# Kernel optimization log

Measured on AMD Instinct MI355X. Metric: run time of the kernel, lower is better.

Reference implementation:

```python
import jax, jax.numpy as jnp
import numpy as np

B, L, D, H, BS, R, MLP = 2, 4096, 768, 12, 64, 3, 3072
HD = D // H            # 64 head dim
NB = L // BS           # 64 blocks
EPS = 1e-6
SEED = 0               # connectivity_seed


def _rand_plan():
    """Static BigBird key-block plan for middle query blocks: [NB-2, 5+R].
    Columns: global first, global last, window (i-1, i, i+1), R random blocks."""
    rng = np.random.RandomState(SEED)
    rows = []
    for i in range(1, NB - 1):
        excl = {0, NB - 1, i - 1, i, i + 1}
        cand = np.array([j for j in range(NB) if j not in excl])
        rnd = rng.choice(cand, size=R, replace=False)
        rows.append(np.concatenate([np.array([0, NB - 1, i - 1, i, i + 1]), rnd]))
    return jnp.asarray(np.stack(rows), dtype=jnp.int32)

_PLAN = _rand_plan()


def _layernorm(x, scale, bias):
    mu = jnp.mean(x, axis=-1, keepdims=True)
    var = jnp.mean(jnp.square(x - mu), axis=-1, keepdims=True)
    return (x - mu) * jax.lax.rsqrt(var + EPS) * scale + bias


def _bigbird_attention(x, Wq, Wk, Wv, Wo):
    # projections: [B,L,D] x [D,H,HD] -> [B,H,L,HD]; flax scales q by 1/sqrt(HD)
    q = jnp.einsum('bld,dhk->bhlk', x, Wq) / jnp.sqrt(jnp.asarray(HD, x.dtype))
    k = jnp.einsum('bld,dhk->bhlk', x, Wk)
    v = jnp.einsum('bld,dhk->bhlk', x, Wv)
    qb = q.reshape(B, H, NB, BS, HD)
    kb = k.reshape(B, H, NB, BS, HD)
    vb = v.reshape(B, H, NB, BS, HD)
    # global query rows (first & last block) attend densely to all keys
    qg = qb[:, :, jnp.array([0, NB - 1])]                 # [B,H,2,BS,HD]
    sg = jnp.einsum('bhgqd,bhld->bhgql', qg, k)           # [B,H,2,BS,L]
    og = jnp.einsum('bhgql,bhld->bhgqd', jax.nn.softmax(sg, axis=-1), v)
    # middle query rows: gather window + global + random key blocks
    S = _PLAN.shape[1]                                     # 5 + R = 8 blocks
    km = kb[:, :, _PLAN].reshape(B, H, NB - 2, S * BS, HD)
    vm = vb[:, :, _PLAN].reshape(B, H, NB - 2, S * BS, HD)
    sm = jnp.einsum('bhmqd,bhmkd->bhmqk', qb[:, :, 1:NB - 1], km)
    om = jnp.einsum('bhmqk,bhmkd->bhmqd', jax.nn.softmax(sm, axis=-1), vm)
    ob = jnp.concatenate([og[:, :, :1], om, og[:, :, 1:]], axis=2)  # [B,H,NB,BS,HD]
    o = ob.reshape(B, H, L, HD)
    return jnp.einsum('bhlk,hkd->bld', o, Wo)


def setup_inputs() -> dict:
    key = jax.random.key(0)
    ks = jax.random.split(key, 8)
    s_qkv = (2.0 / (D + HD)) ** 0.5   # xavier-uniform-ish std
    s_mlp1 = (2.0 / (D + MLP)) ** 0.5
    return {
        'x': jax.random.normal(ks[0], (B, L, D), jnp.float32),
        'ln1_scale': jnp.ones((D,), jnp.float32),
        'ln1_bias': jnp.zeros((D,), jnp.float32),
        'Wq': jax.random.normal(ks[1], (D, H, HD), jnp.float32) * s_qkv,
        'Wk': jax.random.normal(ks[2], (D, H, HD), jnp.float32) * s_qkv,
        'Wv': jax.random.normal(ks[3], (D, H, HD), jnp.float32) * s_qkv,
        'Wo': jax.random.normal(ks[4], (H, HD, D), jnp.float32) * s_qkv,
        'ln2_scale': jnp.ones((D,), jnp.float32),
        'ln2_bias': jnp.zeros((D,), jnp.float32),
        'W1': jax.random.normal(ks[5], (D, MLP), jnp.float32) * s_mlp1,
        'b1': jnp.zeros((MLP,), jnp.float32),
        'W2': jax.random.normal(ks[6], (MLP, D), jnp.float32) * s_mlp1,
        'b2': jnp.zeros((D,), jnp.float32),
    }


def reference(x, ln1_scale, ln1_bias, Wq, Wk, Wv, Wo, ln2_scale, ln2_bias, W1, b1, W2, b2):
    h = _layernorm(x, ln1_scale, ln1_bias)
    attn = _bigbird_attention(h, Wq, Wk, Wv, Wo)
    x1 = attn + x                                  # residual (dropout deterministic)
    y = _layernorm(x1, ln2_scale, ln2_bias)
    y = jax.nn.relu(jnp.einsum('bld,df->blf', y, W1) + b1)
    y = jnp.einsum('blf,fd->bld', y, W2) + b2
    return x1 + y
```

## Files before the change

kernel.cpp:

```cpp
#include <hip/hip_runtime.h>
#include <stdint.h>

constexpr int D_MODEL = 768;
constexpr int SEQ     = 4096;
constexpr int NHEAD   = 12;
constexpr int HDIM    = 64;
constexpr int BATCH   = 2;
constexpr int DFF     = 3072;
constexpr int ROWS    = BATCH * SEQ;

typedef __attribute__((ext_vector_type(8))) __bf16 bfrag;
typedef __attribute__((ext_vector_type(8))) short  s16x8;
typedef __attribute__((ext_vector_type(4))) short  s16x4;
typedef __attribute__((ext_vector_type(4))) float  f32x4;

#define MFMA16(a, b, c) __builtin_amdgcn_mfma_f32_16x16x32_bf16((a), (b), (c), 0, 0, 0)
#define AS1(p) ((__attribute__((address_space(1))) void*)(uintptr_t)(p))
#define AS3(p) ((__attribute__((address_space(3))) void*)(p))

__device__ __forceinline__ float b2f(short s) {
  union { unsigned u; float f; } c;
  c.u = ((unsigned)(unsigned short)s) << 16;
  return c.f;
}
__device__ __forceinline__ short f2b(float f) {
  union { float f; unsigned u; } c;
  c.f = f;
  unsigned r = c.u + 0x7fffu + ((c.u >> 16) & 1u);
  return (short)(r >> 16);
}

struct PlanT { int v[64][8]; };

struct MTRng {
  unsigned mt[624];
  int mti;
  constexpr MTRng() : mt{}, mti(624) {
    mt[0] = 0u;
    for (int i = 1; i < 624; ++i)
      mt[i] = 1812433253u * (mt[i-1] ^ (mt[i-1] >> 30)) + (unsigned)i;
  }
  constexpr unsigned next() {
    if (mti >= 624) {
      for (int i = 0; i < 624; ++i) {
        unsigned y = (mt[i] & 0x80000000u) | (mt[(i+1) % 624] & 0x7fffffffu);
        unsigned v = mt[(i+397) % 624] ^ (y >> 1);
        if (y & 1u) v ^= 0x9908b0dfu;
        mt[i] = v;
      }
      mti = 0;
    }
    unsigned y = mt[mti++];
    y ^= y >> 11;
    y ^= (y << 7)  & 0x9d2c5680u;
    y ^= (y << 15) & 0xefc60000u;
    y ^= y >> 18;
    return y;
  }
  constexpr unsigned interval(unsigned mx) {
    unsigned mask = mx;
    mask |= mask >> 1; mask |= mask >> 2; mask |= mask >> 4;
    mask |= mask >> 8; mask |= mask >> 16;
    unsigned v = next() & mask;
    while (v > mx) v = next() & mask;
    return v;
  }
};

constexpr PlanT make_plan() {
  PlanT P{};
  MTRng rng{};
  for (int i = 1; i <= 62; ++i) {
    int cand[64] = {}; int n = 0;
    for (int j = 0; j < 64; ++j) {
      if (j == 0 || j == 63 || j == i-1 || j == i || j == i+1) continue;
      cand[n++] = j;
    }
    int perm[64] = {};
    for (int p = 0; p < n; ++p) perm[p] = p;
    for (int p = n - 1; p > 0; --p) {
      int j = (int)rng.interval((unsigned)p);
      int t = perm[p]; perm[p] = perm[j]; perm[j] = t;
    }
    P.v[i][0] = 0;  P.v[i][1] = 63; P.v[i][2] = i-1; P.v[i][3] = i; P.v[i][4] = i+1;
    P.v[i][5] = cand[perm[0]]; P.v[i][6] = cand[perm[1]]; P.v[i][7] = cand[perm[2]];
  }
  return P;
}
constexpr PlanT h_plan = make_plan();
__constant__ PlanT g_plan = h_plan;

__global__ __launch_bounds__(256) void ln_kernel(
    const float* __restrict__ x, const float* __restrict__ sc,
    const float* __restrict__ bi, short* __restrict__ y)
{
  const int row = blockIdx.x, tid = threadIdx.x;
  const size_t base = (size_t)row * D_MODEL;
  float v0 = x[base + tid], v1 = x[base + tid + 256], v2 = x[base + tid + 512];
  float s  = v0 + v1 + v2;
  float s2 = v0*v0 + v1*v1 + v2*v2;
  for (int off = 1; off < 64; off <<= 1) {
    s  += __shfl_xor(s,  off);
    s2 += __shfl_xor(s2, off);
  }
  __shared__ float red[8];
  if ((tid & 63) == 0) { red[tid >> 6] = s; red[4 + (tid >> 6)] = s2; }
  __syncthreads();
  s  = red[0] + red[1] + red[2] + red[3];
  s2 = red[4] + red[5] + red[6] + red[7];
  const float mu  = s * (1.f / 768.f);
  const float var = s2 * (1.f / 768.f) - mu * mu;
  const float rs  = rsqrtf(var + 1e-6f);
  short* yr = y + base;
  yr[tid]       = f2b((v0 - mu) * rs * sc[tid]       + bi[tid]);
  yr[tid + 256] = f2b((v1 - mu) * rs * sc[tid + 256] + bi[tid + 256]);
  yr[tid + 512] = f2b((v2 - mu) * rs * sc[tid + 512] + bi[tid + 512]);
}

struct TrArgs { const float* src[6]; short* dst[6]; };

__global__ __launch_bounds__(256) void tr_all(TrArgs a) {
  __shared__ short tile[32][33];
  const int idx = blockIdx.x;
  int w, bx, by, Rr, Cc;
  if (idx < 2304)      { w = idx / 576; int t = idx % 576;  bx = t % 24; by = t / 24; Rr = 768;  Cc = 768;  }
  else if (idx < 4608) { w = 4;         int t = idx - 2304; bx = t % 96; by = t / 96; Rr = 768;  Cc = 3072; }
  else                 { w = 5;         int t = idx - 4608; bx = t % 24; by = t / 24; Rr = 3072; Cc = 768;  }
  const float* in = a.src[w];
  short* out = a.dst[w];
  const int x0 = bx * 32, y0 = by * 32;
  const int tx = threadIdx.x & 31, ty = threadIdx.x >> 5;
  for (int i = 0; i < 32; i += 8)
    tile[ty + i][tx] = f2b(in[(size_t)(y0 + ty + i) * Cc + x0 + tx]);
  __syncthreads();
  for (int i = 0; i < 32; i += 8)
    out[(size_t)(x0 + ty + i) * Rr + y0 + tx] = tile[tx][ty + i];
}

enum { M_QKV = 0, M_RES = 3, M_BRELU = 4, M_BRES = 5 };

template <int MODE, int TN>
__global__ __launch_bounds__(256) void gemm_bt(
    const short* __restrict__ A, const short* __restrict__ Bt,
    void* __restrict__ Cv, short* __restrict__ C2, short* __restrict__ C3,
    const float* __restrict__ res, const float* __restrict__ bias, int N, int K)
{
  constexpr int NT = TN / 32;
  alignas(16) __shared__ short As[3][128 * 32];
  alignas(16) __shared__ short Bs[3][TN * 32];
  const int tid = threadIdx.x;
  const int wave = tid >> 6, lane = tid & 63;
  const int quad = lane >> 4, l15 = lane & 15;
  const int m0 = blockIdx.x * 128, n0 = blockIdx.y * TN;
  const int mw = (wave & 1) * 64, nw = (wave >> 1) * (TN / 2);

  f32x4 acc[4][NT];
#pragma unroll
  for (int i = 0; i < 4; ++i)
#pragma unroll
    for (int j = 0; j < NT; ++j) acc[i][j] = f32x4{0.f, 0.f, 0.f, 0.f};

  const int srow = wave * 32 + (lane >> 2);
  const int scol = (lane & 3) * 8;
  const size_t arow = (size_t)(m0 + srow) * K + scol;
  const size_t brow128 = (size_t)(n0 + srow) * K + scol;
  const size_t brow64  = (size_t)(n0 + wave * 16 + (lane >> 2)) * K + scol;

  auto STAGE = [&](int buf, int k0) {
    __builtin_amdgcn_global_load_lds(AS1(A + arow + k0),                AS3(As[buf] + (wave*32     ) * 32), 16, 0, 0);
    __builtin_amdgcn_global_load_lds(AS1(A + arow + k0 + (size_t)16*K), AS3(As[buf] + (wave*32 + 16) * 32), 16, 0, 0);
    if constexpr (TN == 128) {
      __builtin_amdgcn_global_load_lds(AS1(Bt + brow128 + k0),                AS3(Bs[buf] + (wave*32     ) * 32), 16, 0, 0);
      __builtin_amdgcn_global_load_lds(AS1(Bt + brow128 + k0 + (size_t)16*K), AS3(Bs[buf] + (wave*32 + 16) * 32), 16, 0, 0);
    } else {
      __builtin_amdgcn_global_load_lds(AS1(Bt + brow64 + k0), AS3(Bs[buf] + (wave*16) * 32), 16, 0, 0);
    }
  };

  STAGE(0, 0);

  int cb = 0;
  for (int k0 = 0; k0 < K; k0 += 32) {
    const int kn = k0 + 32;
    int sb = cb + 1; if (sb >= 3) sb -= 3;
    __builtin_amdgcn_sched_barrier(0);
    STAGE(sb, kn < K ? kn : 0);
    if constexpr (TN == 128) asm volatile("s_waitcnt vmcnt(4)" ::: "memory");
    else                     asm volatile("s_waitcnt vmcnt(3)" ::: "memory");
    __builtin_amdgcn_s_barrier();
    __builtin_amdgcn_sched_barrier(0);

    bfrag af[4], bfv[NT];
#pragma unroll
    for (int mt = 0; mt < 4; ++mt)  af[mt]  = *(const bfrag*)(As[cb] + (mw + mt*16 + l15) * 32 + quad * 8);
#pragma unroll
    for (int nt = 0; nt < NT; ++nt) bfv[nt] = *(const bfrag*)(Bs[cb] + (nw + nt*16 + l15) * 32 + quad * 8);
#pragma unroll
    for (int mt = 0; mt < 4; ++mt)
#pragma unroll
      for (int nt = 0; nt < NT; ++nt)
        acc[mt][nt] = MFMA16(af[mt], bfv[nt], acc[mt][nt]);

    cb = sb;
  }
  asm volatile("s_waitcnt vmcnt(0)" ::: "memory");

#pragma unroll
  for (int mt = 0; mt < 4; ++mt) {
#pragma unroll
    for (int nt = 0; nt < NT; ++nt) {
      if (MODE == M_QKV) {
        const int gn = n0 + nw + nt*16 + l15;
        const int seg = gn / 768, gn2 = gn - seg * 768;
        const int gm0 = m0 + mw + mt*16 + quad*4;
        if (seg == 2) {
          const int bb = gm0 >> 12, l = gm0 & 4095, hh = gn2 >> 6, hd = gn2 & 63;
          s16x4 pk{f2b(acc[mt][nt][0]), f2b(acc[mt][nt][1]),
                   f2b(acc[mt][nt][2]), f2b(acc[mt][nt][3])};
          *(s16x4*)(&C3[(((size_t)(bb * NHEAD + hh)) * HDIM + hd) * SEQ + l]) = pk;
        } else {
#pragma unroll
          for (int r = 0; r < 4; ++r) {
            const float v = acc[mt][nt][r];
            if (seg == 0) ((short*)Cv)[(size_t)(gm0 + r) * 768 + gn2] = f2b(v * 0.125f);
            else          C2[(size_t)(gm0 + r) * 768 + gn2] = f2b(v);
          }
        }
      } else {
#pragma unroll
        for (int r = 0; r < 4; ++r) {
          const int gm = m0 + mw + mt*16 + quad*4 + r;
          const int gn = n0 + nw + nt*16 + l15;
          float v = acc[mt][nt][r];
          const size_t ci = (size_t)gm * N + gn;
          if (MODE == M_RES)   { ((float*)Cv)[ci] = v + res[ci]; }
          if (MODE == M_BRELU) { v += bias[gn]; ((short*)Cv)[ci] = f2b(v > 0.f ? v : 0.f); }
          if (MODE == M_BRES)  { ((float*)Cv)[ci] = v + bias[gn] + res[ci]; }
        }
      }
    }
  }
}

constexpr int PSTR = 72;
constexpr int KSTR = 68;

__global__ __launch_bounds__(256, 3) void attn_kernel(
    const short* __restrict__ q, const short* __restrict__ k,
    const short* __restrict__ vt, short* __restrict__ o,
    short* __restrict__ Opart, float* __restrict__ ml)
{
  alignas(16) __shared__ short KV[4][64 * KSTR];
  alignas(16) __shared__ short Pbuf[4][2 * 16 * PSTR];
  const int xi = blockIdx.x, h = blockIdx.y, b = blockIdx.z;
  const int tid = threadIdx.x, wave = tid >> 6, lane = tid & 63;
  const int quad = lane >> 4, l15 = lane & 15;
  const int r8 = lane >> 3, g8 = lane & 7;

  int qb, part = 0, g = 0;
  bool partial;
  if (xi < 62) { qb = xi + 1; partial = false; }
  else { const int t = xi - 62; g = t >> 3; part = t & 7; qb = g ? 63 : 0; partial = true; }

  const short* qp = q + (size_t)(b * SEQ + qb * 64 + wave * 16 + l15) * D_MODEL + h * HDIM;
  const bfrag qf0 = *(const bfrag*)(qp + quad * 8);
  const bfrag qf1 = *(const bfrag*)(qp + 32 + quad * 8);

  const short* kb_base = k  + (size_t)b * SEQ * D_MODEL + h * HDIM;
  const short* vt_base = vt + ((size_t)(b * NHEAD + h)) * HDIM * SEQ;

  const int sr0 = wave * 16 + r8, sr1 = wave * 16 + 8 + r8;

  auto kidx = [&](int t, int which) -> int {
    const int tt = t > 3 ? 3 : t;
    return partial ? (part * 8 + 2 * tt + which) : g_plan.v[qb][2 * tt + which];
  };
  auto load8 = [&](int k0i, int k1i, s16x8* R) {
    const short* ka = kb_base + (size_t)k0i * 64 * D_MODEL + g8 * 8;
    const short* kbp = kb_base + (size_t)k1i * 64 * D_MODEL + g8 * 8;
    const short* va = vt_base + (size_t)k0i * 64 + g8 * 8;
    const short* vb = vt_base + (size_t)k1i * 64 + g8 * 8;
    R[0] = *(const s16x8*)(ka  + (size_t)sr0 * D_MODEL);
    R[1] = *(const s16x8*)(ka  + (size_t)sr1 * D_MODEL);
    R[2] = *(const s16x8*)(kbp + (size_t)sr0 * D_MODEL);
    R[3] = *(const s16x8*)(kbp + (size_t)sr1 * D_MODEL);
    R[4] = *(const s16x8*)(va  + (size_t)sr0 * SEQ);
    R[5] = *(const s16x8*)(va  + (size_t)sr1 * SEQ);
    R[6] = *(const s16x8*)(vb  + (size_t)sr0 * SEQ);
    R[7] = *(const s16x8*)(vb  + (size_t)sr1 * SEQ);
  };

  float m_r[4], l_r[4];
  f32x4 oacc[4];
#pragma unroll
  for (int r = 0; r < 4; ++r) { m_r[r] = -1e9f; l_r[r] = 0.f; }
#pragma unroll
  for (int nt = 0; nt < 4; ++nt) oacc[nt] = f32x4{0.f, 0.f, 0.f, 0.f};

  short* pb = &Pbuf[wave][0];

  s16x8 R[8];
  load8(kidx(0, 0), kidx(0, 1), R);

  for (int it = 0; it < 4; ++it) {
    __syncthreads();
#pragma unroll
    for (int bu = 0; bu < 4; ++bu) {
      *(s16x8*)(&KV[bu][sr0 * KSTR + g8 * 8]) = R[2 * bu];
      *(s16x8*)(&KV[bu][sr1 * KSTR + g8 * 8]) = R[2 * bu + 1];
    }
    __syncthreads();

    load8(kidx(it + 1, 0), kidx(it + 1, 1), R);

    f32x4 s0[4], s1[4];
#pragma unroll
    for (int nt = 0; nt < 4; ++nt) {
      const int fr = (nt * 16 + l15) * KSTR + quad * 8;
      const bfrag ka0 = *(const bfrag*)(&KV[0][fr]);
      const bfrag ka1 = *(const bfrag*)(&KV[0][fr + 32]);
      const bfrag kb0 = *(const bfrag*)(&KV[1][fr]);
      const bfrag kb1 = *(const bfrag*)(&KV[1][fr + 32]);
      s0[nt] = f32x4{0.f,0.f,0.f,0.f}; s1[nt] = f32x4{0.f,0.f,0.f,0.f};
      s0[nt] = MFMA16(qf0, ka0, s0[nt]); s0[nt] = MFMA16(qf1, ka1, s0[nt]);
      s1[nt] = MFMA16(qf0, kb0, s1[nt]); s1[nt] = MFMA16(qf1, kb1, s1[nt]);
    }

    float alpha[4];
#pragma unroll
    for (int r = 0; r < 4; ++r) {
      float v = fmaxf(fmaxf(fmaxf(s0[0][r], s0[1][r]), fmaxf(s0[2][r], s0[3][r])),
                      fmaxf(fmaxf(s1[0][r], s1[1][r]), fmaxf(s1[2][r], s1[3][r])));
      v = fmaxf(v, __shfl_xor(v, 1));
      v = fmaxf(v, __shfl_xor(v, 2));
      v = fmaxf(v, __shfl_xor(v, 4));
      v = fmaxf(v, __shfl_xor(v, 8));
      const float mn = fmaxf(m_r[r], v);
      alpha[r] = __expf(m_r[r] - mn);
      m_r[r] = mn;
    }
    float psum[4] = {0.f, 0.f, 0.f, 0.f};
#pragma unroll
    for (int nt = 0; nt < 4; ++nt)
#pragma unroll
      for (int r = 0; r < 4; ++r) {
        const float p0 = __expf(s0[nt][r] - m_r[r]);
        const float p1 = __expf(s1[nt][r] - m_r[r]);
        s0[nt][r] = p0; s1[nt][r] = p1;
        psum[r] += p0 + p1;
      }
#pragma unroll
    for (int r = 0; r < 4; ++r) {
      float v = psum[r];
      v += __shfl_xor(v, 1); v += __shfl_xor(v, 2);
      v += __shfl_xor(v, 4); v += __shfl_xor(v, 8);
      l_r[r] = l_r[r] * alpha[r] + v;
    }

#pragma unroll
    for (int nt = 0; nt < 4; ++nt)
#pragma unroll
      for (int r = 0; r < 4; ++r) {
        pb[(quad * 4 + r) * PSTR + nt * 16 + l15]             = f2b(s0[nt][r]);
        pb[16 * PSTR + (quad * 4 + r) * PSTR + nt * 16 + l15] = f2b(s1[nt][r]);
      }

#pragma unroll
    for (int nt = 0; nt < 4; ++nt)
#pragma unroll
      for (int r = 0; r < 4; ++r) oacc[nt][r] *= alpha[r];
#pragma unroll
    for (int s = 0; s < 2; ++s) {
      const bfrag pf0 = *(const bfrag*)(pb + l15 * PSTR + s * 32 + quad * 8);
      const bfrag pf1 = *(const bfrag*)(pb + 16 * PSTR + l15 * PSTR + s * 32 + quad * 8);
#pragma unroll
      for (int nt = 0; nt < 4; ++nt) {
        const int fr = (nt * 16 + l15) * KSTR + s * 32 + quad * 8;
        const bfrag vf0 = *(const bfrag*)(&KV[2][fr]);
        const bfrag vf1 = *(const bfrag*)(&KV[3][fr]);
        oacc[nt] = MFMA16(pf0, vf0, oacc[nt]);
        oacc[nt] = MFMA16(pf1, vf1, oacc[nt]);
      }
    }
  }

  if (!partial) {
    short* op = o + (size_t)(b * SEQ + qb * 64 + wave * 16) * D_MODEL + h * HDIM;
#pragma unroll
    for (int r = 0; r < 4; ++r) {
      const float inv = 1.f / l_r[r];
#pragma unroll
      for (int nt = 0; nt < 4; ++nt)
        op[(size_t)(quad * 4 + r) * D_MODEL + nt * 16 + l15] = f2b(oacc[nt][r] * inv);
    }
  } else {
    const int pi = ((b * NHEAD + h) * 2 + g) * 8 + part;
    short* Op = Opart + (size_t)pi * 4096;
    float* mp = ml + (size_t)pi * 128;
#pragma unroll
    for (int r = 0; r < 4; ++r) {
      const int row = wave * 16 + quad * 4 + r;
#pragma unroll
      for (int nt = 0; nt < 4; ++nt)
        Op[row * 64 + nt * 16 + l15] = f2b(oacc[nt][r]);
      if (l15 == 0) { mp[row] = m_r[r]; mp[64 + row] = l_r[r]; }
    }
  }
}

__global__ __launch_bounds__(256) void attn_merge(
    const short* __restrict__ Opart, const float* __restrict__ ml,
    short* __restrict__ o)
{
  const int bi = blockIdx.x;
  const int g = bi & 1, h = (bi >> 1) % NHEAD, b = bi / (2 * NHEAD);
  const int qb = g ? 63 : 0;
  const int pi0 = bi * 8;
#pragma unroll
  for (int e = 0; e < 16; ++e) {
    const int idx = threadIdx.x + e * 256;
    const int r = idx >> 6, c = idx & 63;
    float ms = -1e9f;
#pragma unroll
    for (int p = 0; p < 8; ++p) ms = fmaxf(ms, ml[(size_t)(pi0 + p) * 128 + r]);
    float lsum = 0.f, osum = 0.f;
#pragma unroll
    for (int p = 0; p < 8; ++p) {
      const float w = __expf(ml[(size_t)(pi0 + p) * 128 + r] - ms);
      lsum += w * ml[(size_t)(pi0 + p) * 128 + 64 + r];
      osum += w * b2f(Opart[(size_t)(pi0 + p) * 4096 + idx]);
    }
    o[(size_t)(b * SEQ + qb * 64 + r) * D_MODEL + h * HDIM + c] = f2b(osum / lsum);
  }
}

extern "C" void kernel_launch(void* const* d_in, const int* in_sizes, int n_in,
                              void* d_out, int out_size, void* d_ws, size_t ws_size,
                              hipStream_t stream) {
  (void)in_sizes; (void)n_in; (void)out_size; (void)ws_size;
  const float* x    = (const float*)d_in[0];
  const float* ln1s = (const float*)d_in[1];
  const float* ln1b = (const float*)d_in[2];
  const float* Wq   = (const float*)d_in[3];
  const float* Wk   = (const float*)d_in[4];
  const float* Wv   = (const float*)d_in[5];
  const float* Wo   = (const float*)d_in[6];
  const float* ln2s = (const float*)d_in[7];
  const float* ln2b = (const float*)d_in[8];
  const float* W1   = (const float*)d_in[9];
  const float* b1   = (const float*)d_in[10];
  const float* W2   = (const float*)d_in[11];
  const float* b2   = (const float*)d_in[12];
  float* out = (float*)d_out;

  short* WqT  = (short*)((char*)d_ws + 256);
  short* WkT  = WqT  + 768 * 768;
  short* WvT  = WkT  + 768 * 768;
  short* WoT  = WvT  + 768 * 768;
  short* W1T  = WoT  + 768 * 768;
  short* W2T  = W1T  + (size_t)3072 * 768;
  short* hbuf = W2T  + (size_t)3072 * 768;
  short* qbuf = hbuf + (size_t)ROWS * D_MODEL;
  short* kbuf = qbuf + (size_t)ROWS * D_MODEL;
  short* vtb  = kbuf + (size_t)ROWS * D_MODEL;
  short* obuf = vtb  + (size_t)ROWS * D_MODEL;
  short* tbuf = qbuf;
  short* Opart = hbuf;
  float* mlbuf = (float*)(hbuf + (size_t)384 * 4096);

  TrArgs ta;
  ta.src[0] = Wq; ta.src[1] = Wk; ta.src[2] = Wv; ta.src[3] = Wo; ta.src[4] = W1; ta.src[5] = W2;
  ta.dst[0] = WqT; ta.dst[1] = WkT; ta.dst[2] = WvT; ta.dst[3] = WoT; ta.dst[4] = W1T; ta.dst[5] = W2T;
  tr_all<<<6912, 256, 0, stream>>>(ta);

  ln_kernel<<<ROWS, 256, 0, stream>>>(x, ln1s, ln1b, hbuf);

  gemm_bt<M_QKV, 128><<<dim3(64, 18), 256, 0, stream>>>(hbuf, WqT, qbuf, kbuf, vtb, nullptr, nullptr, 2304, 768);

  attn_kernel<<<dim3(78, 12, 2), 256, 0, stream>>>(qbuf, kbuf, vtb, obuf, Opart, mlbuf);
  attn_merge<<<48, 256, 0, stream>>>(Opart, mlbuf, obuf);

  gemm_bt<M_RES, 64><<<dim3(64, 12), 256, 0, stream>>>(obuf, WoT, out, nullptr, nullptr, x, nullptr, 768, 768);

  ln_kernel<<<ROWS, 256, 0, stream>>>(out, ln2s, ln2b, hbuf);

  gemm_bt<M_BRELU, 128><<<dim3(64, 24), 256, 0, stream>>>(hbuf, W1T, tbuf, nullptr, nullptr, nullptr, b1, 3072, 768);
  gemm_bt<M_BRES, 64> <<<dim3(64, 12), 256, 0, stream>>>(tbuf, W2T, out, nullptr, nullptr, out, b2, 768, 3072);
}
```

Baseline: 354.3 us.

## Deepen TN=64 GEMM pipeline with 4-stage LDS ring and register double-buffering

For the TN=64 GEMM variant, the LDS ring buffer grows from 3 to 4 stages and global loads are issued two k-tiles ahead. The main loop is unrolled by two, with A and B fragments ping-ponged between two register sets. Each iteration's LDS reads for the next tile are overlapped with the MFMAs on the current tile. This is meant to hide LDS-read and global-load latency, at the cost of more LDS per block, more registers, and an assumption that K/32 is even.

```diff
diff --git a/kernel.cpp b/kernel.cpp
--- a/kernel.cpp
+++ b/kernel.cpp
@@ -145,9 +145,10 @@
     void* __restrict__ Cv, short* __restrict__ C2, short* __restrict__ C3,
     const float* __restrict__ res, const float* __restrict__ bias, int N, int K)
 {
-  constexpr int NT = TN / 32;
-  alignas(16) __shared__ short As[3][128 * 32];
-  alignas(16) __shared__ short Bs[3][TN * 32];
+  constexpr int NT    = TN / 32;
+  constexpr int DEPTH = (TN == 64) ? 4 : 3;
+  alignas(16) __shared__ short As[DEPTH][128 * 32];
+  alignas(16) __shared__ short Bs[DEPTH][TN * 32];
   const int tid = threadIdx.x;
   const int wave = tid >> 6, lane = tid & 63;
   const int quad = lane >> 4, l15 = lane & 15;
@@ -177,33 +178,88 @@
     }
   };
 
-  STAGE(0, 0);
-
-  int cb = 0;
-  for (int k0 = 0; k0 < K; k0 += 32) {
-    const int kn = k0 + 32;
-    int sb = cb + 1; if (sb >= 3) sb -= 3;
-    __builtin_amdgcn_sched_barrier(0);
-    STAGE(sb, kn < K ? kn : 0);
-    if constexpr (TN == 128) asm volatile("s_waitcnt vmcnt(4)" ::: "memory");
-    else                     asm volatile("s_waitcnt vmcnt(3)" ::: "memory");
+  if constexpr (TN == 64) {
+    STAGE(0, 0);
+    STAGE(1, 32);
+    asm volatile("s_waitcnt vmcnt(3)" ::: "memory");
     __builtin_amdgcn_s_barrier();
     __builtin_amdgcn_sched_barrier(0);
 
-    bfrag af[4], bfv[NT];
-#pragma unroll
-    for (int mt = 0; mt < 4; ++mt)  af[mt]  = *(const bfrag*)(As[cb] + (mw + mt*16 + l15) * 32 + quad * 8);
-#pragma unroll
-    for (int nt = 0; nt < NT; ++nt) bfv[nt] = *(const bfrag*)(Bs[cb] + (nw + nt*16 + l15) * 32 + quad * 8);
-#pragma unroll
-    for (int mt = 0; mt < 4; ++mt)
-#pragma unroll
-      for (int nt = 0; nt < NT; ++nt)
-        acc[mt][nt] = MFMA16(af[mt], bfv[nt], acc[mt][nt]);
-
-    cb = sb;
-  }
-  asm volatile("s_waitcnt vmcnt(0)" ::: "memory");
+    bfrag afA[4], bfA[2], afB[4], bfB[2];
+#pragma unroll
+    for (int mt = 0; mt < 4; ++mt) afA[mt] = *(const bfrag*)(As[0] + (mw + mt*16 + l15) * 32 + quad * 8);
+#pragma unroll
+    for (int nt = 0; nt < 2; ++nt) bfA[nt] = *(const bfrag*)(Bs[0] + (nw + nt*16 + l15) * 32 + quad * 8);
+
+    const int NK = K >> 5;
+    for (int kt = 0; kt < NK; kt += 2) {
+      {
+        const int k2 = (kt + 2) * 32;
+        __builtin_amdgcn_sched_barrier(0);
+        STAGE((kt + 2) & 3, k2 < K ? k2 : 0);
+        asm volatile("s_waitcnt vmcnt(3)" ::: "memory");
+        __builtin_amdgcn_s_barrier();
+        __builtin_amdgcn_sched_barrier(0);
+        const short* an = As[(kt + 1) & 3];
+        const short* bn = Bs[(kt + 1) & 3];
+#pragma unroll
+        for (int mt = 0; mt < 4; ++mt) afB[mt] = *(const bfrag*)(an + (mw + mt*16 + l15) * 32 + quad * 8);
+#pragma unroll
+        for (int nt = 0; nt < 2; ++nt) bfB[nt] = *(const bfrag*)(bn + (nw + nt*16 + l15) * 32 + quad * 8);
+#pragma unroll
+        for (int mt = 0; mt < 4; ++mt)
+#pragma unroll
+          for (int nt = 0; nt < 2; ++nt)
+            acc[mt][nt] = MFMA16(afA[mt], bfA[nt], acc[mt][nt]);
+      }
+      {
+        const int k2 = (kt + 3) * 32;
+        __builtin_amdgcn_sched_barrier(0);
+        STAGE((kt + 3) & 3, k2 < K ? k2 : 0);
+        asm volatile("s_waitcnt vmcnt(3)" ::: "memory");
+        __builtin_amdgcn_s_barrier();
+        __builtin_amdgcn_sched_barrier(0);
+        const short* an = As[(kt + 2) & 3];
+        const short* bn = Bs[(kt + 2) & 3];
+#pragma unroll
+        for (int mt = 0; mt < 4; ++mt) afA[mt] = *(const bfrag*)(an + (mw + mt*16 + l15) * 32 + quad * 8);
+#pragma unroll
+        for (int nt = 0; nt < 2; ++nt) bfA[nt] = *(const bfrag*)(bn + (nw + nt*16 + l15) * 32 + quad * 8);
+#pragma unroll
+        for (int mt = 0; mt < 4; ++mt)
+#pragma unroll
+          for (int nt = 0; nt < 2; ++nt)
+            acc[mt][nt] = MFMA16(afB[mt], bfB[nt], acc[mt][nt]);
+      }
+    }
+    asm volatile("s_waitcnt vmcnt(0)" ::: "memory");
+  } else {
+    STAGE(0, 0);
+    int cb = 0;
+    for (int k0 = 0; k0 < K; k0 += 32) {
+      const int kn = k0 + 32;
+      int sb = cb + 1; if (sb >= 3) sb -= 3;
+      __builtin_amdgcn_sched_barrier(0);
+      STAGE(sb, kn < K ? kn : 0);
+      asm volatile("s_waitcnt vmcnt(4)" ::: "memory");
+      __builtin_amdgcn_s_barrier();
+      __builtin_amdgcn_sched_barrier(0);
+
+      bfrag af[4], bfv[NT];
+#pragma unroll
+      for (int mt = 0; mt < 4; ++mt)  af[mt]  = *(const bfrag*)(As[cb] + (mw + mt*16 + l15) * 32 + quad * 8);
+#pragma unroll
+      for (int nt = 0; nt < NT; ++nt) bfv[nt] = *(const bfrag*)(Bs[cb] + (nw + nt*16 + l15) * 32 + quad * 8);
+#pragma unroll
+      for (int mt = 0; mt < 4; ++mt)
+#pragma unroll
+        for (int nt = 0; nt < NT; ++nt)
+          acc[mt][nt] = MFMA16(af[mt], bfv[nt], acc[mt][nt]);
+
+      cb = sb;
+    }
+    asm volatile("s_waitcnt vmcnt(0)" ::: "memory");
+  }
 
 #pragma unroll
   for (int mt = 0; mt < 4; ++mt) {
```

Result: slower. 363.5 us (+2.6%).
